# Performance work log

Hardware: AMD Instinct MI355X
Metric: run time of the kernel (lower is better)

The kernel has to match this reference:

```python
import jax, jax.numpy as jnp
import numpy as np

N_NODES = 100000


def gcn_conv(x, edge_index, W, b):
    # PyG GCNConv: add self-loops, symmetric normalization D^-1/2 (A+I) D^-1/2, then linear.
    n = x.shape[0]
    loop = jnp.arange(n, dtype=edge_index.dtype)
    src = jnp.concatenate([edge_index[0], loop])
    dst = jnp.concatenate([edge_index[1], loop])
    deg = jax.ops.segment_sum(jnp.ones_like(dst, dtype=x.dtype), dst, num_segments=n)
    dinv = jnp.where(deg > 0, jax.lax.rsqrt(deg), 0.0)
    norm = dinv[src] * dinv[dst]                      # [E+N]
    h = x @ W                                          # [N, out]
    msg = h[src] * norm[:, None]                       # gather + scale
    out = jax.ops.segment_sum(msg, dst, num_segments=n)  # scatter-add
    return out + b


def forward_one(x, edge_index, W1, b1, W2, b2, fc_w, fc_b):
    x = jax.nn.relu(gcn_conv(x, edge_index, W1, b1))
    x = jax.nn.relu(gcn_conv(x, edge_index, W2, b2))
    x = jnp.mean(x, axis=0)                            # [hidden]
    return x @ fc_w.T + fc_b


def setup_inputs() -> dict:
    key = jax.random.key(0)
    ks = jax.random.split(key, 10)
    d_in, d_h = 64, 64
    E = 1600000
    s = 1.0 / np.sqrt(d_in)
    return {
        "x1": jax.random.normal(ks[0], (N_NODES, d_in), jnp.float32),
        "x2": jax.random.normal(ks[1], (N_NODES, d_in), jnp.float32),
        "edge_index1": jax.random.randint(ks[2], (2, E), 0, N_NODES, jnp.int32),
        "edge_index2": jax.random.randint(ks[3], (2, E), 0, N_NODES, jnp.int32),
        "W1": jax.random.normal(ks[4], (d_in, d_h), jnp.float32) * s,
        "b1": jnp.zeros((d_h,), jnp.float32),
        "W2": jax.random.normal(ks[5], (d_h, d_h), jnp.float32) * s,
        "b2": jnp.zeros((d_h,), jnp.float32),
        "fc_w": jax.random.normal(ks[6], (d_h, d_h), jnp.float32) * s,
        "fc_b": jnp.zeros((d_h,), jnp.float32),
    }


def reference(x1, x2, edge_index1, edge_index2, W1, b1, W2, b2, fc_w, fc_b):
    out1 = forward_one(x1, edge_index1, W1, b1, W2, b2, fc_w, fc_b)
    out2 = forward_one(x2, edge_index2, W1, b1, W2, b2, fc_w, fc_b)
    return (out1, out2)
```

## Files before the change

kernel.cpp:

```cpp
#include <hip/hip_runtime.h>


#define TPB    256
#define CHUNK  128
#define SHIFT  7
#define KMAX   1024
#define CAP    2560
#define EPB    8192
#define CPAD   16

typedef __attribute__((ext_vector_type(8))) short short8;
typedef __attribute__((ext_vector_type(4))) float f32x4;
typedef __attribute__((ext_vector_type(2))) float float2v;
typedef __attribute__((ext_vector_type(2))) unsigned int uint2v;

struct Ctx {
    const float* X; const int* esrc; const int* edst;
    unsigned int* temp; unsigned char* Hs2; unsigned char* Hs;
    unsigned int* csr; int* row_ptr; int* degA; float* dinv; int* cursorG;
    float* P; float* P2; float* outp;
};

__device__ __forceinline__ unsigned short f2bf(float x) {
    union { float f; unsigned int i; } c; c.f = x;
    unsigned int r = c.i + 0x7FFFu + ((c.i >> 16) & 1u);
    return (unsigned short)(r >> 16);
}
__device__ __forceinline__ unsigned char f2fp8(float x) {
    int p = __builtin_amdgcn_cvt_pk_fp8_f32(x, x, 0, false);
    return (unsigned char)(p & 0xFF);
}
__device__ __forceinline__ float2v up8lo(unsigned int w) {
    return __builtin_amdgcn_cvt_pk_f32_fp8(w, false);
}
__device__ __forceinline__ float2v up8hi(unsigned int w) {
    return __builtin_amdgcn_cvt_pk_f32_fp8(w, true);
}

__global__ void k_prepW2(const float* __restrict__ W1, const float* __restrict__ W2,
                         unsigned short* __restrict__ Wt1, unsigned short* __restrict__ Wt2) {
    const float* W = blockIdx.x ? W2 : W1;
    unsigned short* Wt = blockIdx.x ? Wt2 : Wt1;
    for (int i = threadIdx.x; i < 64 * 64; i += 256) {
        int n = i >> 6, k = i & 63;
        Wt[i] = f2bf(W[k * 64 + n]);
    }
}

__global__ void k_zeroCur(Ctx c0, Ctx c1, int nb0, int K, int N) {
    int b = blockIdx.x; Ctx c = c0;
    if (b >= nb0) { c = c1; b -= nb0; }
    int i = b * blockDim.x + threadIdx.x;
    if (i < K) c.cursorG[i * CPAD] = 0;
    if (b == 0 && threadIdx.x < 64) c.Hs[(size_t)N * 64 + threadIdx.x] = 0;
}

__global__ __launch_bounds__(1024) void k_binA(Ctx c0, Ctx c1, int nb0, int E, int K) {
    __shared__ int cnt[KMAX];
    __shared__ int ofs[KMAX];
    __shared__ int segBase[KMAX];
    __shared__ int wsum[16];
    __shared__ unsigned int sorted[EPB];
    __shared__ unsigned short bkt[EPB];
    int b = blockIdx.x; Ctx c = c0;
    if (b >= nb0) { c = c1; b -= nb0; }
    int tid = threadIdx.x;
    cnt[tid] = 0;
    __syncthreads();
    int base = b * EPB;
    int tot = E - base; if (tot > EPB) tot = EPB;
    int rd[EPB / 1024];
    unsigned int rs[EPB / 1024];
#pragma unroll
    for (int k = 0; k < EPB / 1024; ++k) {
        int e = base + k * 1024 + tid;
        rd[k] = -1; rs[k] = 0;
        if (e < E) {
            rd[k] = c.edst[e];
            rs[k] = (unsigned int)c.esrc[e];
            atomicAdd(&cnt[rd[k] >> SHIFT], 1);
        }
    }
    __syncthreads();
    int v = cnt[tid];
    int lane = tid & 63, w = tid >> 6;
    int x = v;
#pragma unroll
    for (int off = 1; off < 64; off <<= 1) {
        int t = __shfl_up(x, off, 64);
        if (lane >= off) x += t;
    }
    if (lane == 63) wsum[w] = x;
    __syncthreads();
    if (tid < 16) {
        int y = wsum[tid];
#pragma unroll
        for (int off = 1; off < 16; off <<= 1) {
            int t = __shfl_up(y, off, 16);
            if ((tid & 15) >= off) y += t;
        }
        wsum[tid] = y;
    }
    __syncthreads();
    int pre = w ? wsum[w - 1] : 0;
    ofs[tid] = x + pre - v;
    if (tid < K) {
        segBase[tid] = v ? atomicAdd(&c.cursorG[tid * CPAD], v) : 0;
    } else {
        segBase[tid] = 0;
    }
    cnt[tid] = 0;
    __syncthreads();
#pragma unroll
    for (int k = 0; k < EPB / 1024; ++k) {
        if (rd[k] >= 0) {
            int bk = rd[k] >> SHIFT;
            int r = atomicAdd(&cnt[bk], 1);
            int p = ofs[bk] + r;
            sorted[p] = ((unsigned int)(rd[k] & (CHUNK - 1)) << 17) | rs[k];
            bkt[p] = (unsigned short)bk;
        }
    }
    __syncthreads();
    for (int p = tid; p < tot; p += 1024) {
        unsigned int vv = sorted[p];
        int bk = bkt[p];
        int pos = segBase[bk] + (p - ofs[bk]);
        if (pos < CAP) c.temp[(size_t)bk * CAP + pos] = vv;
    }
}

__global__ __launch_bounds__(256) void k_csrb(Ctx c0, Ctx c1, int nb0, int N) {
    __shared__ int deg[CHUNK];
    __shared__ int lofs[CHUNK];
    __shared__ int cur[CHUNK];
    __shared__ int wsum2[2];
    __shared__ unsigned int tl[CAP];
    int b = blockIdx.x; Ctx c = c0;
    if (b >= nb0) { c = c1; b -= nb0; }
    int tid = threadIdx.x;
    if (tid < CHUNK) deg[tid] = 0;
    __syncthreads();
    int cnt = c.cursorG[b * CPAD]; if (cnt > CAP) cnt = CAP;
    const size_t tb = (size_t)b * CAP;
    for (int i = tid; i < cnt; i += 256) {
        unsigned int vv = c.temp[tb + i];
        tl[i] = vv;
        atomicAdd(&deg[vv >> 17], 1);
    }
    __syncthreads();
    int vdeg = 0, x = 0;
    if (tid < CHUNK) { vdeg = deg[tid]; x = vdeg; }
#pragma unroll
    for (int off = 1; off < 64; off <<= 1) {
        int t = __shfl_up(x, off, 64);
        if ((tid & 63) >= off) x += t;
    }
    if (tid < CHUNK && (tid & 63) == 63) wsum2[tid >> 6] = x;
    __syncthreads();
    int base = b * CAP;
    if (tid < CHUNK) {
        int pre = (tid >> 6) ? wsum2[0] : 0;
        int excl = x + pre - vdeg;
        lofs[tid] = excl;
        cur[tid] = 0;
        int node = b * CHUNK + tid;
        if (node < N) {
            c.row_ptr[node] = base + excl;
            c.degA[node] = vdeg;
            c.dinv[node] = rsqrtf((float)vdeg + 1.0f);
        }
    }
    __syncthreads();
    for (int i = tid; i < cnt; i += 256) {
        unsigned int p = tl[i];
        int dl = p >> 17;
        int rank = atomicAdd(&cur[dl], 1);
        c.csr[base + lofs[dl] + rank] = (p & 0x1FFFFu) << 6;
    }
}

__device__ __forceinline__ void mfma_tail(short8 a0, short8 a1,
                                          const unsigned short* __restrict__ Wt,
                                          unsigned char* __restrict__ Hs,
                                          int row0, int r, int q, int N) {
    short8 bfrag[4][2];
#pragma unroll
    for (int ct = 0; ct < 4; ++ct)
#pragma unroll
        for (int kb = 0; kb < 2; ++kb)
            bfrag[ct][kb] = *(const short8*)(Wt + (ct * 16 + r) * 64 + q * 8 + 32 * kb);
    f32x4 acc[4];
#pragma unroll
    for (int ct = 0; ct < 4; ++ct) {
        acc[ct] = (f32x4){0.0f, 0.0f, 0.0f, 0.0f};
        acc[ct] = __builtin_amdgcn_mfma_f32_16x16x32_bf16(a0, bfrag[ct][0], acc[ct], 0, 0, 0);
        acc[ct] = __builtin_amdgcn_mfma_f32_16x16x32_bf16(a1, bfrag[ct][1], acc[ct], 0, 0, 0);
    }
#pragma unroll
    for (int reg = 0; reg < 4; ++reg) {
        int row = row0 + q * 4 + reg;
        if (row < N) {
            size_t base = (size_t)row * 64 + r;
#pragma unroll
            for (int ct = 0; ct < 4; ++ct)
                Hs[base + ct * 16] = f2fp8(acc[ct][reg]);
        }
    }
}

__global__ __launch_bounds__(256) void k_gemm1(Ctx c0, Ctx c1, int nb0,
                                               const unsigned short* __restrict__ Wt,
                                               int nTiles, int N) {
    int b = blockIdx.x; Ctx c = c0;
    if (b >= nb0) { c = c1; b -= nb0; }
    int wave = threadIdx.x >> 6, lane = threadIdx.x & 63;
    int tile = b * 4 + wave;
    if (tile >= nTiles) return;
    int r = lane & 15, q = lane >> 4;
    int row0 = tile * 16;
    int row = row0 + r;
    int rr = row < N ? row : N - 1;
    float d = c.dinv[rr];
    const float* xrow = c.X + (size_t)rr * 64 + q * 8;
    short8 a0, a1;
#pragma unroll
    for (int j = 0; j < 8; ++j) a0[j] = (short)f2bf(xrow[j] * d);
#pragma unroll
    for (int j = 0; j < 8; ++j) a1[j] = (short)f2bf(xrow[32 + j] * d);
    mfma_tail(a0, a1, Wt, c.Hs, row0, r, q, N);
}

__device__ __forceinline__ void agg_map(int bi, int nb0, int swz,
                                        const Ctx& c0, const Ctx& c1,
                                        Ctx& c, int& b) {
    if (swz) {
        int graph = (bi >> 2) & 1;
        b = ((bi >> 3) << 2) | (bi & 3);
        c = graph ? c1 : c0;
    } else {
        b = bi; c = c0;
        if (b >= nb0) { c = c1; b -= nb0; }
    }
}

__device__ __forceinline__ void agg_issue8w(const unsigned char* __restrict__ Hs,
                                            unsigned int idx, int lim,
                                            int hbase, int j, unsigned int s8,
                                            uint2v* h) {
#pragma unroll
    for (int u = 0; u < 8; ++u) {
        if (4 * u >= lim) break;
        unsigned int su = (unsigned int)__shfl((int)idx, hbase + 4 * u + j, 64);
        h[u] = *(const uint2v*)(Hs + (su | s8));
    }
}
__device__ __forceinline__ void agg_cons8w(const uint2v* h, int lim, float2v* acc) {
#pragma unroll
    for (int u = 0; u < 8; ++u) {
        if (4 * u >= lim) break;
        acc[0] += up8lo(h[u][0]); acc[1] += up8hi(h[u][0]);
        acc[2] += up8lo(h[u][1]); acc[3] += up8hi(h[u][1]);
    }
}

__device__ __forceinline__ void agg_pair2(const unsigned char* __restrict__ Hs,
                                          const unsigned int* __restrict__ csr,
                                          int beg0, int deg0, int maxs0,
                                          int beg1, int deg1, int maxs1,
                                          int lane, unsigned int sent,
                                          float2v* acc0, float2v* acc1) {
    int hbase = lane & 32;
    int hl = lane & 31;
    int j = (hl >> 3) & 3;
    unsigned int s8 = (unsigned int)((lane & 7) * 8);
    unsigned int idx0 = (hl < deg0) ? csr[beg0 + hl] : sent;
    unsigned int idx1 = (hl < deg1) ? csr[beg1 + hl] : sent;
    int lim0 = maxs0 > 32 ? 32 : maxs0;
    int lim1 = maxs1 > 32 ? 32 : maxs1;
    uint2v h0[8], h1[8];
    agg_issue8w(Hs, idx0, lim0, hbase, j, s8, h0);
    agg_issue8w(Hs, idx1, lim1, hbase, j, s8, h1);
    agg_cons8w(h0, lim0, acc0);
    agg_cons8w(h1, lim1, acc1);
    for (int base = 32; base < maxs0; base += 32) {
        unsigned int idx = (base + hl < deg0) ? csr[beg0 + base + hl] : sent;
        int lim = maxs0 - base; if (lim > 32) lim = 32;
        uint2v hh[8];
        agg_issue8w(Hs, idx, lim, hbase, j, s8, hh);
        agg_cons8w(hh, lim, acc0);
    }
    for (int base = 32; base < maxs1; base += 32) {
        unsigned int idx = (base + hl < deg1) ? csr[beg1 + base + hl] : sent;
        int lim = maxs1 - base; if (lim > 32) lim = 32;
        uint2v hh[8];
        agg_issue8w(Hs, idx, lim, hbase, j, s8, hh);
        agg_cons8w(hh, lim, acc1);
    }
#pragma unroll
    for (int k = 0; k < 4; ++k) {
        float2v o;
        o.x = __shfl_xor(acc0[k].x, 8, 64);  o.y = __shfl_xor(acc0[k].y, 8, 64);
        acc0[k] += o;
        o.x = __shfl_xor(acc0[k].x, 16, 64); o.y = __shfl_xor(acc0[k].y, 16, 64);
        acc0[k] += o;
        o.x = __shfl_xor(acc1[k].x, 8, 64);  o.y = __shfl_xor(acc1[k].y, 8, 64);
        acc1[k] += o;
        o.x = __shfl_xor(acc1[k].x, 16, 64); o.y = __shfl_xor(acc1[k].y, 16, 64);
        acc1[k] += o;
    }
}

__global__ __launch_bounds__(256, 8) void k_agg1(Ctx c0, Ctx c1, int nb0, int swz,
                                                 const float* __restrict__ bias,
                                                 const unsigned short* __restrict__ Wt2,
                                                 int n) {
    __shared__ unsigned short As[16][64];
    Ctx c; int b;
    agg_map(blockIdx.x, nb0, swz, c0, c1, c, b);
    int wave = threadIdx.x >> 6, lane = threadIdx.x & 63;
    int h = lane >> 5;
    int nbase = b * 16 + wave * 4;
    int node0 = nbase + h;
    int node1 = nbase + 2 + h;
    int nd0 = node0 < n ? node0 : 0;
    int nd1 = node1 < n ? node1 : 0;
    int beg0 = c.row_ptr[nd0];
    int beg1 = c.row_ptr[nd1];
    int deg0 = (node0 < n) ? c.degA[nd0] : 0;
    int deg1 = (node1 < n) ? c.degA[nd1] : 0;
    int od0 = __shfl_xor(deg0, 32, 64); int m0 = deg0 > od0 ? deg0 : od0;
    int od1 = __shfl_xor(deg1, 32, 64); int m1 = deg1 > od1 ? deg1 : od1;
    int maxs0 = __builtin_amdgcn_readfirstlane(m0);
    int maxs1 = __builtin_amdgcn_readfirstlane(m1);
    if (b == 0 && threadIdx.x < 64) c.Hs2[(size_t)n * 64 + threadIdx.x] = 0;
    float2v acc0[4] = {{0.f,0.f},{0.f,0.f},{0.f,0.f},{0.f,0.f}};
    float2v acc1[4] = {{0.f,0.f},{0.f,0.f},{0.f,0.f},{0.f,0.f}};
    agg_pair2(c.Hs, c.csr, beg0, deg0, maxs0, beg1, deg1, maxs1,
              lane, (unsigned int)n << 6, acc0, acc1);
    if (((lane >> 3) & 3) == 0) {
        int s = lane & 7;
#pragma unroll
        for (int pr = 0; pr < 2; ++pr) {
            const float2v* ac = pr ? acc1 : acc0;
            int node = nbase + pr * 2 + h;
            ushort4 oA = {0, 0, 0, 0}, oB = {0, 0, 0, 0};
            if (node < n) {
                uint2v hv = *(const uint2v*)(c.Hs + (size_t)node * 64 + s * 8);
                float2v h0 = up8lo(hv[0]), h1 = up8hi(hv[0]);
                float2v h2 = up8lo(hv[1]), h3 = up8hi(hv[1]);
                float4 ba = *(const float4*)(bias + s * 8);
                float4 bb = *(const float4*)(bias + s * 8 + 4);
                float d = c.dinv[node];
                oA.x = f2bf(fmaxf(ba.x + d * (ac[0].x + h0.x), 0.0f) * d);
                oA.y = f2bf(fmaxf(ba.y + d * (ac[0].y + h0.y), 0.0f) * d);
                oA.z = f2bf(fmaxf(ba.z + d * (ac[1].x + h1.x), 0.0f) * d);
                oA.w = f2bf(fmaxf(ba.w + d * (ac[1].y + h1.y), 0.0f) * d);
                oB.x = f2bf(fmaxf(bb.x + d * (ac[2].x + h2.x), 0.0f) * d);
                oB.y = f2bf(fmaxf(bb.y + d * (ac[2].y + h2.y), 0.0f) * d);
                oB.z = f2bf(fmaxf(bb.z + d * (ac[3].x + h3.x), 0.0f) * d);
                oB.w = f2bf(fmaxf(bb.w + d * (ac[3].y + h3.y), 0.0f) * d);
            }
            int row = wave * 4 + pr * 2 + h;
            int col = (s * 8) ^ ((row & 7) << 3);
            *(ushort4*)(&As[row][col]) = oA;
            *(ushort4*)(&As[row][col + 4]) = oB;
        }
    }
    __syncthreads();
    {
        int r = lane & 15, q = lane >> 4;
        int sw = (r & 7) << 3;
        short8 a0 = *(const short8*)(&As[r][(q * 8) ^ sw]);
        short8 a1 = *(const short8*)(&As[r][(q * 8 + 32) ^ sw]);
        const unsigned short* wp = Wt2 + (wave * 16 + r) * 64 + q * 8;
        short8 b0 = *(const short8*)(wp);
        short8 b1 = *(const short8*)(wp + 32);
        f32x4 acc2 = {0.0f, 0.0f, 0.0f, 0.0f};
        acc2 = __builtin_amdgcn_mfma_f32_16x16x32_bf16(a0, b0, acc2, 0, 0, 0);
        acc2 = __builtin_amdgcn_mfma_f32_16x16x32_bf16(a1, b1, acc2, 0, 0, 0);
#pragma unroll
        for (int reg = 0; reg < 4; ++reg) {
            int l = q * 4 + reg;
            int row = b * 16 + l;
            if (row < n)
                c.Hs2[(size_t)row * 64 + wave * 16 + r] = f2fp8(acc2[reg]);
        }
    }
}

__global__ __launch_bounds__(256, 8) void k_agg2(Ctx c0, Ctx c1, int nb0, int swz,
                                                 const float* __restrict__ bias, int n) {
    __shared__ float red[16 * 64];
    Ctx c; int b;
    agg_map(blockIdx.x, nb0, swz, c0, c1, c, b);
    int wave = threadIdx.x >> 6, lane = threadIdx.x & 63;
    int h = lane >> 5;
    int nbase = b * 16 + wave * 4;
    int node0 = nbase + h;
    int node1 = nbase + 2 + h;
    int nd0 = node0 < n ? node0 : 0;
    int nd1 = node1 < n ? node1 : 0;
    int beg0 = c.row_ptr[nd0];
    int beg1 = c.row_ptr[nd1];
    int deg0 = (node0 < n) ? c.degA[nd0] : 0;
    int deg1 = (node1 < n) ? c.degA[nd1] : 0;
    int od0 = __shfl_xor(deg0, 32, 64); int m0 = deg0 > od0 ? deg0 : od0;
    int od1 = __shfl_xor(deg1, 32, 64); int m1 = deg1 > od1 ? deg1 : od1;
    int maxs0 = __builtin_amdgcn_readfirstlane(m0);
    int maxs1 = __builtin_amdgcn_readfirstlane(m1);
    float2v acc0[4] = {{0.f,0.f},{0.f,0.f},{0.f,0.f},{0.f,0.f}};
    float2v acc1[4] = {{0.f,0.f},{0.f,0.f},{0.f,0.f},{0.f,0.f}};
    agg_pair2(c.Hs2, c.csr, beg0, deg0, maxs0, beg1, deg1, maxs1,
              lane, (unsigned int)n << 6, acc0, acc1);
    if (((lane >> 3) & 3) == 0) {
        int s = lane & 7;
#pragma unroll
        for (int pr = 0; pr < 2; ++pr) {
            const float2v* ac = pr ? acc1 : acc0;
            int node = nbase + pr * 2 + h;
            float4 vA = {0.f, 0.f, 0.f, 0.f}, vB = {0.f, 0.f, 0.f, 0.f};
            if (node < n) {
                uint2v hv = *(const uint2v*)(c.Hs2 + (size_t)node * 64 + s * 8);
                float2v h0 = up8lo(hv[0]), h1 = up8hi(hv[0]);
                float2v h2 = up8lo(hv[1]), h3 = up8hi(hv[1]);
                float4 ba = *(const float4*)(bias + s * 8);
                float4 bb = *(const float4*)(bias + s * 8 + 4);
                float d = c.dinv[node];
                vA.x = fmaxf(ba.x + d * (ac[0].x + h0.x), 0.0f);
                vA.y = fmaxf(ba.y + d * (ac[0].y + h0.y), 0.0f);
                vA.z = fmaxf(ba.z + d * (ac[1].x + h1.x), 0.0f);
                vA.w = fmaxf(ba.w + d * (ac[1].y + h1.y), 0.0f);
                vB.x = fmaxf(bb.x + d * (ac[2].x + h2.x), 0.0f);
                vB.y = fmaxf(bb.y + d * (ac[2].y + h2.y), 0.0f);
                vB.z = fmaxf(bb.z + d * (ac[3].x + h3.x), 0.0f);
                vB.w = fmaxf(bb.w + d * (ac[3].y + h3.y), 0.0f);
            }
            int row = wave * 4 + pr * 2 + h;
            *(float4*)(&red[row * 64 + s * 8]) = vA;
            *(float4*)(&red[row * 64 + s * 8 + 4]) = vB;
        }
    }
    __syncthreads();
    if (threadIdx.x < 64) {
        float acc16 = 0.0f;
#pragma unroll
        for (int r = 0; r < 16; ++r) acc16 += red[r * 64 + threadIdx.x];
        c.P[(size_t)b * 64 + threadIdx.x] = acc16;
    }
}

__global__ void k_colsum(Ctx c0, Ctx c1, int nb0, int rows) {
    int b = blockIdx.x; Ctx c = c0;
    if (b >= nb0) { c = c1; b -= nb0; }
    int f = threadIdx.x;
    float acc = 0.0f;
    for (int r = b; r < rows; r += nb0) acc += c.P[(size_t)r * 64 + f];
    c.P2[b * 64 + f] = acc;
}

__global__ void k_fc(Ctx c0, Ctx c1, const float* __restrict__ fcw,
                     const float* __restrict__ fcb, int n) {
    Ctx c = blockIdx.x ? c1 : c0;
    __shared__ float S[64];
    int j = threadIdx.x;
    float s = 0.0f;
    for (int r = 0; r < 256; ++r) s += c.P2[r * 64 + j];
    S[j] = s;
    __syncthreads();
    float inv = 1.0f / (float)n;
    float acc = fcb[j];
#pragma unroll
    for (int k = 0; k < 64; ++k) acc += (S[k] * inv) * fcw[j * 64 + k];
    c.outp[j] = acc;
}

extern "C" void kernel_launch(void* const* d_in, const int* in_sizes, int n_in,
                              void* d_out, int out_size, void* d_ws, size_t ws_size,
                              hipStream_t stream) {
    const float* x[2]  = {(const float*)d_in[0], (const float*)d_in[1]};
    const int*   ei[2] = {(const int*)d_in[2], (const int*)d_in[3]};
    const float* W1  = (const float*)d_in[4];
    const float* b1  = (const float*)d_in[5];
    const float* W2  = (const float*)d_in[6];
    const float* b2  = (const float*)d_in[7];
    const float* fcw = (const float*)d_in[8];
    const float* fcb = (const float*)d_in[9];
    float* out = (float*)d_out;

    const int N  = in_sizes[0] / 64;
    const int E  = in_sizes[2] / 2;
    const int NF = N * 64;
    const int K  = (N + CHUNK - 1) / CHUNK;
    const int gGm  = (N + 15) / 16;
    const int gGmP = (gGm + 3) & ~3;
    const int nTiles = (N + 15) / 16;
    const int gMf = (nTiles + 3) / 4;
    const int gBin = (E + EPB - 1) / EPB;
    const int gK  = (K + TPB - 1) / TPB;

    auto al = [](size_t x) { return (x + 127) & ~(size_t)127; };
    size_t tempB = (size_t)K * CAP * 4;
    size_t hs2B  = (size_t)NF + 64;
    size_t szRegion = al(tempB > hs2B ? tempB : hs2B);
    size_t szHs  = al((size_t)NF + 64);
    size_t szCsr = al((size_t)K * CAP * 4);
    size_t szRp  = al((size_t)N * 4);
    size_t szDeg = al((size_t)N * 4);
    size_t szDi  = al((size_t)N * 4);
    size_t szCu  = al((size_t)K * CPAD * 4);
    size_t szP   = al((size_t)gGmP * 64 * 4);
    size_t szP2  = al((size_t)256 * 64 * 4);
    size_t setB  = szRegion + szHs + szCsr + szRp + szDeg + szDi + szCu + szP + szP2;
    size_t wtB   = 2 * al(64 * 64 * 2);
    bool batched = ws_size >= wtB + 2 * setB;

    char* base = (char*)d_ws;
    unsigned short* Wt1 = (unsigned short*)base;
    unsigned short* Wt2 = (unsigned short*)(base + al(64 * 64 * 2));

    auto mkctx = [&](int g, char* p) {
        Ctx c;
        c.X = x[g]; c.esrc = ei[g]; c.edst = ei[g] + E;
        c.temp = (unsigned int*)p; c.Hs2 = (unsigned char*)p; p += szRegion;
        c.Hs = (unsigned char*)p; p += szHs;
        c.csr = (unsigned int*)p; p += szCsr;
        c.row_ptr = (int*)p; p += szRp;
        c.degA = (int*)p; p += szDeg;
        c.dinv = (float*)p; p += szDi;
        c.cursorG = (int*)p; p += szCu;
        c.P = (float*)p; p += szP;
        c.P2 = (float*)p;
        c.outp = out + g * 64;
        return c;
    };
    char* set0 = base + wtB;
    Ctx c0 = mkctx(0, set0);
    Ctx c1 = mkctx(1, batched ? set0 + setB : set0);

    k_prepW2<<<2, 256, 0, stream>>>(W1, W2, Wt1, Wt2);

    auto pipe = [&](Ctx A, Ctx B, int mult) {
        int swz = (mult == 2) ? 1 : 0;
        k_zeroCur<<<mult * gK, TPB, 0, stream>>>(A, B, gK, K, N);
        k_binA<<<mult * gBin, 1024, 0, stream>>>(A, B, gBin, E, K);
        k_csrb<<<mult * K, 256, 0, stream>>>(A, B, K, N);
        k_gemm1<<<mult * gMf, 256, 0, stream>>>(A, B, gMf, Wt1, nTiles, N);
        k_agg1<<<mult * gGmP, 256, 0, stream>>>(A, B, gGmP, swz, b1, Wt2, N);
        k_agg2<<<mult * gGmP, 256, 0, stream>>>(A, B, gGmP, swz, b2, N);
        k_colsum<<<mult * 256, 64, 0, stream>>>(A, B, 256, gGmP);
        k_fc<<<mult, 64, 0, stream>>>(A, B, fcw, fcb, N);
    };

    if (batched) {
        pipe(c0, c1, 2);
    } else {
        pipe(c0, c0, 1);
        pipe(c1, c1, 1);
    }
}
```

Measured before the change: 278.7 us.

## Fuse first GEMM into CSR build, reuse atomic ranks, drop colsum kernel

The layer-1 GEMM is folded into the CSR build kernel, which now uses dinv from shared memory and handles its own 128-node chunk. Each edge's local atomic rank is kept from the counting pass, so the second atomic pass in both binning and CSR build goes away. The per-block partial sums in agg2 are atomically accumulated into a 512-row buffer that k_zeroCur zeroes, and the colsum kernel is removed with k_fc doing the final reduction over 256 threads. This cuts two launches and some atomics in exchange for more work per CSR block and global float atomics, which make the summation order nondeterministic.

Measured after the change: 302.6 us. 1.09x slower.

```diff
diff --git a/kernel.cpp b/kernel.cpp
--- a/kernel.cpp
+++ b/kernel.cpp
@@ -8,6 +8,7 @@
 #define CAP    2560
 #define EPB    8192
 #define CPAD   16
+#define P2R    512
 
 typedef __attribute__((ext_vector_type(8))) short short8;
 typedef __attribute__((ext_vector_type(4))) float f32x4;
@@ -18,7 +19,7 @@
     const float* X; const int* esrc; const int* edst;
     unsigned int* temp; unsigned char* Hs2; unsigned char* Hs;
     unsigned int* csr; int* row_ptr; int* degA; float* dinv; int* cursorG;
-    float* P; float* P2; float* outp;
+    float* P2; float* outp;
 };
 
 __device__ __forceinline__ unsigned short f2bf(float x) {
@@ -53,6 +54,8 @@
     int i = b * blockDim.x + threadIdx.x;
     if (i < K) c.cursorG[i * CPAD] = 0;
     if (b == 0 && threadIdx.x < 64) c.Hs[(size_t)N * 64 + threadIdx.x] = 0;
+    int stride = nb0 * blockDim.x;
+    for (int j = i; j < P2R * 64; j += stride) c.P2[j] = 0.0f;
 }
 
 __global__ __launch_bounds__(1024) void k_binA(Ctx c0, Ctx c1, int nb0, int E, int K) {
@@ -69,16 +72,17 @@
     __syncthreads();
     int base = b * EPB;
     int tot = E - base; if (tot > EPB) tot = EPB;
-    int rd[EPB / 1024];
+    unsigned int rd[EPB / 1024];
     unsigned int rs[EPB / 1024];
 #pragma unroll
     for (int k = 0; k < EPB / 1024; ++k) {
         int e = base + k * 1024 + tid;
-        rd[k] = -1; rs[k] = 0;
+        rd[k] = 0xFFFFFFFFu; rs[k] = 0;
         if (e < E) {
-            rd[k] = c.edst[e];
+            unsigned int dst = (unsigned int)c.edst[e];
             rs[k] = (unsigned int)c.esrc[e];
-            atomicAdd(&cnt[rd[k] >> SHIFT], 1);
+            unsigned int rk = (unsigned int)atomicAdd(&cnt[dst >> SHIFT], 1);
+            rd[k] = dst | (rk << 17);
         }
     }
     __syncthreads();
@@ -109,15 +113,15 @@
     } else {
         segBase[tid] = 0;
     }
-    cnt[tid] = 0;
     __syncthreads();
 #pragma unroll
     for (int k = 0; k < EPB / 1024; ++k) {
-        if (rd[k] >= 0) {
-            int bk = rd[k] >> SHIFT;
-            int r = atomicAdd(&cnt[bk], 1);
-            int p = ofs[bk] + r;
-            sorted[p] = ((unsigned int)(rd[k] & (CHUNK - 1)) << 17) | rs[k];
+        if (rd[k] != 0xFFFFFFFFu) {
+            unsigned int dst = rd[k] & 0x1FFFFu;
+            int rk = (int)(rd[k] >> 17);
+            int bk = (int)(dst >> SHIFT);
+            int p = ofs[bk] + rk;
+            sorted[p] = ((dst & (CHUNK - 1)) << 17) | rs[k];
             bkt[p] = (unsigned short)bk;
         }
     }
@@ -130,11 +134,42 @@
     }
 }
 
-__global__ __launch_bounds__(256) void k_csrb(Ctx c0, Ctx c1, int nb0, int N) {
+__device__ __forceinline__ void mfma_tail(short8 a0, short8 a1,
+                                          const unsigned short* __restrict__ Wt,
+                                          unsigned char* __restrict__ Hs,
+                                          int row0, int r, int q, int N) {
+    short8 bfrag[4][2];
+#pragma unroll
+    for (int ct = 0; ct < 4; ++ct)
+#pragma unroll
+        for (int kb = 0; kb < 2; ++kb)
+            bfrag[ct][kb] = *(const short8*)(Wt + (ct * 16 + r) * 64 + q * 8 + 32 * kb);
+    f32x4 acc[4];
+#pragma unroll
+    for (int ct = 0; ct < 4; ++ct) {
+        acc[ct] = (f32x4){0.0f, 0.0f, 0.0f, 0.0f};
+        acc[ct] = __builtin_amdgcn_mfma_f32_16x16x32_bf16(a0, bfrag[ct][0], acc[ct], 0, 0, 0);
+        acc[ct] = __builtin_amdgcn_mfma_f32_16x16x32_bf16(a1, bfrag[ct][1], acc[ct], 0, 0, 0);
+    }
+#pragma unroll
+    for (int reg = 0; reg < 4; ++reg) {
+        int row = row0 + q * 4 + reg;
+        if (row < N) {
+            size_t base = (size_t)row * 64 + r;
+#pragma unroll
+            for (int ct = 0; ct < 4; ++ct)
+                Hs[base + ct * 16] = f2fp8(acc[ct][reg]);
+        }
+    }
+}
+
+__global__ __launch_bounds__(256) void k_csrb(Ctx c0, Ctx c1, int nb0,
+                                              const unsigned short* __restrict__ Wt1,
+                                              int N) {
     __shared__ int deg[CHUNK];
     __shared__ int lofs[CHUNK];
-    __shared__ int cur[CHUNK];
     __shared__ int wsum2[2];
+    __shared__ float sdinv[CHUNK];
     __shared__ unsigned int tl[CAP];
     int b = blockIdx.x; Ctx c = c0;
     if (b >= nb0) { c = c1; b -= nb0; }
@@ -143,10 +178,14 @@
     __syncthreads();
     int cnt = c.cursorG[b * CPAD]; if (cnt > CAP) cnt = CAP;
     const size_t tb = (size_t)b * CAP;
-    for (int i = tid; i < cnt; i += 256) {
-        unsigned int vv = c.temp[tb + i];
-        tl[i] = vv;
-        atomicAdd(&deg[vv >> 17], 1);
+    int rkl[(CAP + 255) / 256];
+    {
+        int it = 0;
+        for (int i = tid; i < cnt; i += 256, ++it) {
+            unsigned int vv = c.temp[tb + i];
+            tl[i] = vv;
+            rkl[it] = atomicAdd(&deg[vv >> 17], 1);
+        }
     }
     __syncthreads();
     int vdeg = 0, x = 0;
@@ -163,72 +202,41 @@
         int pre = (tid >> 6) ? wsum2[0] : 0;
         int excl = x + pre - vdeg;
         lofs[tid] = excl;
-        cur[tid] = 0;
+        sdinv[tid] = rsqrtf((float)vdeg + 1.0f);
         int node = b * CHUNK + tid;
         if (node < N) {
             c.row_ptr[node] = base + excl;
             c.degA[node] = vdeg;
-            c.dinv[node] = rsqrtf((float)vdeg + 1.0f);
-        }
-    }
-    __syncthreads();
-    for (int i = tid; i < cnt; i += 256) {
-        unsigned int p = tl[i];
-        int dl = p >> 17;
-        int rank = atomicAdd(&cur[dl], 1);
-        c.csr[base + lofs[dl] + rank] = (p & 0x1FFFFu) << 6;
-    }
-}
-
-__device__ __forceinline__ void mfma_tail(short8 a0, short8 a1,
-                                          const unsigned short* __restrict__ Wt,
-                                          unsigned char* __restrict__ Hs,
-                                          int row0, int r, int q, int N) {
-    short8 bfrag[4][2];
-#pragma unroll
-    for (int ct = 0; ct < 4; ++ct)
-#pragma unroll
-        for (int kb = 0; kb < 2; ++kb)
-            bfrag[ct][kb] = *(const short8*)(Wt + (ct * 16 + r) * 64 + q * 8 + 32 * kb);
-    f32x4 acc[4];
-#pragma unroll
-    for (int ct = 0; ct < 4; ++ct) {
-        acc[ct] = (f32x4){0.0f, 0.0f, 0.0f, 0.0f};
-        acc[ct] = __builtin_amdgcn_mfma_f32_16x16x32_bf16(a0, bfrag[ct][0], acc[ct], 0, 0, 0);
-        acc[ct] = __builtin_amdgcn_mfma_f32_16x16x32_bf16(a1, bfrag[ct][1], acc[ct], 0, 0, 0);
-    }
-#pragma unroll
-    for (int reg = 0; reg < 4; ++reg) {
-        int row = row0 + q * 4 + reg;
-        if (row < N) {
-            size_t base = (size_t)row * 64 + r;
-#pragma unroll
-            for (int ct = 0; ct < 4; ++ct)
-                Hs[base + ct * 16] = f2fp8(acc[ct][reg]);
-        }
-    }
-}
-
-__global__ __launch_bounds__(256) void k_gemm1(Ctx c0, Ctx c1, int nb0,
-                                               const unsigned short* __restrict__ Wt,
-                                               int nTiles, int N) {
-    int b = blockIdx.x; Ctx c = c0;
-    if (b >= nb0) { c = c1; b -= nb0; }
-    int wave = threadIdx.x >> 6, lane = threadIdx.x & 63;
-    int tile = b * 4 + wave;
-    if (tile >= nTiles) return;
+            c.dinv[node] = sdinv[tid];
+        }
+    }
+    __syncthreads();
+    {
+        int it = 0;
+        for (int i = tid; i < cnt; i += 256, ++it) {
+            unsigned int p = tl[i];
+            int dl = p >> 17;
+            c.csr[base + lofs[dl] + rkl[it]] = (p & 0x1FFFFu) << 6;
+        }
+    }
+    int wave = tid >> 6, lane = tid & 63;
     int r = lane & 15, q = lane >> 4;
-    int row0 = tile * 16;
-    int row = row0 + r;
-    int rr = row < N ? row : N - 1;
-    float d = c.dinv[rr];
-    const float* xrow = c.X + (size_t)rr * 64 + q * 8;
-    short8 a0, a1;
-#pragma unroll
-    for (int j = 0; j < 8; ++j) a0[j] = (short)f2bf(xrow[j] * d);
-#pragma unroll
-    for (int j = 0; j < 8; ++j) a1[j] = (short)f2bf(xrow[32 + j] * d);
-    mfma_tail(a0, a1, Wt, c.Hs, row0, r, q, N);
+#pragma unroll
+    for (int tt = 0; tt < 2; ++tt) {
+        int row0 = b * CHUNK + (wave + tt * 4) * 16;
+        if (row0 < N) {
+            int row = row0 + r;
+            int rr = row < N ? row : N - 1;
+            float d = sdinv[rr - b * CHUNK];
+            const float* xrow = c.X + (size_t)rr * 64 + q * 8;
+            short8 a0, a1;
+#pragma unroll
+            for (int j = 0; j < 8; ++j) a0[j] = (short)f2bf(xrow[j] * d);
+#pragma unroll
+            for (int j = 0; j < 8; ++j) a1[j] = (short)f2bf(xrow[32 + j] * d);
+            mfma_tail(a0, a1, Wt1, c.Hs, row0, r, q, N);
+        }
+    }
 }
 
 __device__ __forceinline__ void agg_map(int bi, int nb0, int swz,
@@ -446,33 +454,31 @@
         float acc16 = 0.0f;
 #pragma unroll
         for (int r = 0; r < 16; ++r) acc16 += red[r * 64 + threadIdx.x];
-        c.P[(size_t)b * 64 + threadIdx.x] = acc16;
-    }
-}
-
-__global__ void k_colsum(Ctx c0, Ctx c1, int nb0, int rows) {
-    int b = blockIdx.x; Ctx c = c0;
-    if (b >= nb0) { c = c1; b -= nb0; }
-    int f = threadIdx.x;
-    float acc = 0.0f;
-    for (int r = b; r < rows; r += nb0) acc += c.P[(size_t)r * 64 + f];
-    c.P2[b * 64 + f] = acc;
-}
-
-__global__ void k_fc(Ctx c0, Ctx c1, const float* __restrict__ fcw,
-                     const float* __restrict__ fcb, int n) {
+        atomicAdd(&c.P2[(b & (P2R - 1)) * 64 + threadIdx.x], acc16);
+    }
+}
+
+__global__ __launch_bounds__(256) void k_fc(Ctx c0, Ctx c1,
+                                            const float* __restrict__ fcw,
+                                            const float* __restrict__ fcb, int n) {
     Ctx c = blockIdx.x ? c1 : c0;
-    __shared__ float S[64];
-    int j = threadIdx.x;
+    __shared__ float Sp[4][64];
+    int j = threadIdx.x & 63, g = threadIdx.x >> 6;
     float s = 0.0f;
-    for (int r = 0; r < 256; ++r) s += c.P2[r * 64 + j];
-    S[j] = s;
-    __syncthreads();
-    float inv = 1.0f / (float)n;
-    float acc = fcb[j];
-#pragma unroll
-    for (int k = 0; k < 64; ++k) acc += (S[k] * inv) * fcw[j * 64 + k];
-    c.outp[j] = acc;
+    for (int r = g; r < P2R; r += 4) s += c.P2[r * 64 + j];
+    Sp[g][j] = s;
+    __syncthreads();
+    if (threadIdx.x < 64) {
+        float S = (Sp[0][j] + Sp[1][j]) + (Sp[2][j] + Sp[3][j]);
+        Sp[0][j] = S * (1.0f / (float)n);
+    }
+    __syncthreads();
+    if (threadIdx.x < 64) {
+        float acc = fcb[j];
+#pragma unroll
+        for (int k = 0; k < 64; ++k) acc += Sp[0][k] * fcw[j * 64 + k];
+        c.outp[j] = acc;
+    }
 }
 
 extern "C" void kernel_launch(void* const* d_in, const int* in_sizes, int n_in,
@@ -494,8 +500,6 @@
     const int K  = (N + CHUNK - 1) / CHUNK;
     const int gGm  = (N + 15) / 16;
     const int gGmP = (gGm + 3) & ~3;
-    const int nTiles = (N + 15) / 16;
-    const int gMf = (nTiles + 3) / 4;
     const int gBin = (E + EPB - 1) / EPB;
     const int gK  = (K + TPB - 1) / TPB;
 
@@ -509,9 +513,8 @@
     size_t szDeg = al((size_t)N * 4);
     size_t szDi  = al((size_t)N * 4);
     size_t szCu  = al((size_t)K * CPAD * 4);
-    size_t szP   = al((size_t)gGmP * 64 * 4);
-    size_t szP2  = al((size_t)256 * 64 * 4);
-    size_t setB  = szRegion + szHs + szCsr + szRp + szDeg + szDi + szCu + szP + szP2;
+    size_t szP2  = al((size_t)P2R * 64 * 4);
+    size_t setB  = szRegion + szHs + szCsr + szRp + szDeg + szDi + szCu + szP2;
     size_t wtB   = 2 * al(64 * 64 * 2);
     bool batched = ws_size >= wtB + 2 * setB;
 
@@ -529,7 +532,6 @@
         c.degA = (int*)p; p += szDeg;
         c.dinv = (float*)p; p += szDi;
         c.cursorG = (int*)p; p += szCu;
-        c.P = (float*)p; p += szP;
         c.P2 = (float*)p;
         c.outp = out + g * 64;
         return c;
@@ -544,12 +546,10 @@
         int swz = (mult == 2) ? 1 : 0;
         k_zeroCur<<<mult * gK, TPB, 0, stream>>>(A, B, gK, K, N);
         k_binA<<<mult * gBin, 1024, 0, stream>>>(A, B, gBin, E, K);
-        k_csrb<<<mult * K, 256, 0, stream>>>(A, B, K, N);
-        k_gemm1<<<mult * gMf, 256, 0, stream>>>(A, B, gMf, Wt1, nTiles, N);
+        k_csrb<<<mult * K, 256, 0, stream>>>(A, B, K, Wt1, N);
         k_agg1<<<mult * gGmP, 256, 0, stream>>>(A, B, gGmP, swz, b1, Wt2, N);
         k_agg2<<<mult * gGmP, 256, 0, stream>>>(A, B, gGmP, swz, b2, N);
-        k_colsum<<<mult * 256, 64, 0, stream>>>(A, B, 256, gGmP);
-        k_fc<<<mult, 64, 0, stream>>>(A, B, fcw, fcb, N);
+        k_fc<<<mult, 256, 0, stream>>>(A, B, fcw, fcb, N);
     };
 
     if (batched) {
```
